# Kernel tuning notes

Hardware: AMD Instinct MI355X
Metric: run time of the kernel (lower is better)

The kernel has to match this reference:

```python
import jax, jax.numpy as jnp
import numpy as np
import math

NBINS = 10
POOL = 8


def setup_inputs() -> dict:
    key = jax.random.key(0)
    x = jax.random.normal(key, (32, 1, 512, 512), dtype=jnp.float32)
    return {"x": x}


def _hog(x):
    # Sobel kernels: (out=2, in=1, 3, 3); channel 0 = horizontal, channel 1 = vertical.
    sob = jnp.array([[1., 0., -1.], [2., 0., -2.], [1., 0., -1.]], dtype=x.dtype)
    w = jnp.stack([sob, sob.T])[:, None, :, :]
    gxy = jax.lax.conv_general_dilated(
        x, w, window_strides=(1, 1), padding=((1, 1), (1, 1)),
        rhs_dilation=(1, 1), dimension_numbers=("NCHW", "OIHW", "NCHW"))
    gx, gy = gxy[:, 0], gxy[:, 1]            # (n, h, w)
    mag = jnp.sqrt(gx * gx + gy * gy)        # gxy.norm(dim=1)
    phase = jnp.arctan2(gx, gy)
    phase_int = phase / math.pi * NBINS
    # torch: out.scatter_(1, floor(phase_int).long() % nbins, mag) on a zero tensor.
    # NOTE: the subsequent out.scatter_add(...) in the source is OUT-OF-PLACE and its
    # result is discarded, so only the floor-bin scatter contributes. Reproduced faithfully.
    bins = jnp.mod(jnp.floor(phase_int).astype(jnp.int32), NBINS)  # (n, h, w), in [0, nbins)
    onehot = bins[:, None, :, :] == jnp.arange(NBINS, dtype=jnp.int32)[None, :, None, None]
    out = jnp.where(onehot, mag[:, None, :, :], jnp.zeros((), dtype=x.dtype))  # (n, nbins, h, w)
    # AvgPool2d(pool=8, stride=8, padding=0): h, w divisible by POOL.
    n, nb, h, wd = out.shape
    pooled = out.reshape(n, nb, h // POOL, POOL, wd // POOL, POOL).mean(axis=(3, 5))
    return pooled


def reference(x):
    # Original forward runs under torch.no_grad(); mirror with stop_gradient.
    return _hog(jax.lax.stop_gradient(x))
```

## Files before the change

kernel.cpp:

```cpp
#include <hip/hip_runtime.h>


namespace {
constexpr int H = 512, W = 512, NB = 10;
}

typedef __attribute__((ext_vector_type(2))) float f32x2;

__device__ __forceinline__ f32x2 vfma2(f32x2 a, f32x2 b, f32x2 c) {
#if __has_builtin(__builtin_elementwise_fma)
    return __builtin_elementwise_fma(a, b, c);
#else
    f32x2 r; r.x = fmaf(a.x, b.x, c.x); r.y = fmaf(a.y, b.y, c.y); return r;
#endif
}

__device__ __forceinline__ void load_row(const float* __restrict__ img,
                                         int ry, int x0, bool lok, bool rok,
                                         float (&R)[10]) {
    if (ry >= 0 && ry < H) {
        const float* p = img + (size_t)ry * W + x0;
        R[0] = lok ? p[-1] : 0.0f;
        const float4 a = *reinterpret_cast<const float4*>(p);
        const float4 b = *reinterpret_cast<const float4*>(p + 4);
        R[1] = a.x; R[2] = a.y; R[3] = a.z; R[4] = a.w;
        R[5] = b.x; R[6] = b.y; R[7] = b.z; R[8] = b.w;
        R[9] = rok ? p[8] : 0.0f;
    } else {
#pragma unroll
        for (int i = 0; i < 10; ++i) R[i] = 0.0f;
    }
}

__global__ __launch_bounds__(256) void hog_kernel(const float* __restrict__ xin,
                                                  float* __restrict__ out) {
    const int tid  = threadIdx.x;
    const int wid  = (blockIdx.x << 2) + (tid >> 6);
    const int lane = tid & 63;

    const int c   = lane >> 2;
    const int sub = lane & 3;

    const int cg  = (wid << 4) + c;
    const int n   = cg >> 12;
    const int rem = cg & 4095;
    const int ph  = rem >> 6;
    const int pw  = rem & 63;

    const int x0 = pw * 8;
    const int yb = ph * 8 + sub * 2;

    const float* img = xin + (size_t)n * H * W;
    const bool lok = (pw > 0), rok = (pw < 63);

    const float PI32 = 3.14159274101257324f;
    const float C10  = __fmul_rn(__fdiv_rn(1.0f, PI32), 10.0f);

    const float P0 =  3.1826723f, P1 = -1.0513758f, P2 = 0.5734066f,
                P3 = -0.2709868f, P4 =  0.0663202f;
    const float EPSW = 1.25e-4f;

    f32x2 acc2[5];
#pragma unroll
    for (int p = 0; p < 5; ++p) acc2[p] = (f32x2){0.0f, 0.0f};

    auto deposit = [&](int b, float v) {
        const bool  hi = b >= 5;
        const int   q5 = hi ? (b - 5) : b;
        const f32x2 P  = hi ? (f32x2){0.0f, v} : (f32x2){v, 0.0f};
#pragma unroll
        for (int p = 0; p < 5; ++p) {
            const float g = (q5 == p) ? 1.0f : 0.0f;
            acc2[p] = vfma2(P, (f32x2){g, g}, acc2[p]);
        }
    };

    auto process_row = [&](const float (&T)[10], const float (&M)[10],
                           const float (&B)[10]) {
        float S[10], D[10];
#pragma unroll
        for (int i = 0; i < 10; ++i) {
            S[i] = fmaf(2.0f, M[i], T[i]) + B[i];
            D[i] = T[i] - B[i];
        }
#pragma unroll
        for (int j = 0; j < 8; ++j) {
            const float gx = S[j] - S[j + 2];
            const float gy = fmaf(2.0f, D[j + 1], D[j] + D[j + 2]);

            const float mag = __builtin_amdgcn_sqrtf(gx * gx + gy * gy);

            const float ax  = fabsf(gx);
            const float ay  = __uint_as_float(__float_as_uint(gy) ^
                                              (__float_as_uint(gx) & 0x80000000u));
            const float aay = fabsf(ay);

            const bool  q   = ax > aay;
            const float den = q ? ax : aay;
            const float num = q ? ay : ax;
            const float t   = num * __builtin_amdgcn_rcpf(den);
            const float u   = t * t;
            float p = fmaf(P4, u, P3);
            p = fmaf(p, u, P2);
            p = fmaf(p, u, P1);
            p = fmaf(p, u, P0);
            const float s = t * p;
            const float w = q ? (5.0f - s) : ((ay > 0.0f) ? s : (10.0f - s));

            const float dist = fabsf(w - rintf(w));
            const bool flagged = !(dist >= EPSW);

            int   bi;
            float dep;
            if (!flagged) {
                bi  = (int)w;
                dep = mag;
            } else {
                const float t0 = T[j], t1 = T[j + 1], t2 = T[j + 2];
                const float m0 = M[j],                 m2 = M[j + 2];
                const float b0 = B[j], b1 = B[j + 1], b2 = B[j + 2];
                const float gxs = ((((t0 - t2) + 2.0f * m0) - 2.0f * m2) + b0) - b2;
                const float gys = ((((t0 + 2.0f * t1) + t2) - b0) - 2.0f * b1) - b2;
                const float mgs = __builtin_amdgcn_sqrtf(gxs * gxs + gys * gys);

                const float phs = atan2f(gxs, gys);
                const float w10 = __fmul_rn(phs, C10);
                bi = (int)floorf(w10);
                bi %= 10;
                if (bi < 0) bi += 10;
                float half = 0.0f;
                const float rk  = rintf(w10);
                const float eps = fmaxf(4.0f * fabsf(w10) * 1.1920929e-7f, 1.5e-6f);
                if (fabsf(w10 - rk) < eps && mgs < 4.6f) {
                    const int k  = (int)rk;
                    int kb = k % 10;       if (kb < 0) kb += 10;
                    int ka = (k - 1) % 10; if (ka < 0) ka += 10;
                    const int balt = (bi == kb) ? ka : kb;
                    half = 0.5f * mgs;
                    deposit(balt, half);
                }
                dep = mgs - half;
            }

            deposit(bi, dep);
        }
    };

    float R0[10], R1[10], R2[10], R3[10];
    load_row(img, yb - 1, x0, lok, rok, R0);
    load_row(img, yb,     x0, lok, rok, R1);
    load_row(img, yb + 1, x0, lok, rok, R2);
    load_row(img, yb + 2, x0, lok, rok, R3);
    process_row(R0, R1, R2);
    process_row(R1, R2, R3);

    float v0 = 0.0f, v1 = 0.0f, v2 = 0.0f, v3 = 0.0f, v4 = 0.0f;
#pragma unroll
    for (int p = 0; p < 5; ++p) {
        float sx = acc2[p].x, sy = acc2[p].y;
        sx += __shfl_xor(sx, 1, 64);
        sx += __shfl_xor(sx, 2, 64);
        sy += __shfl_xor(sy, 1, 64);
        sy += __shfl_xor(sy, 2, 64);
        const float vq = (sub & 1) ? sy : sx;
        v0 = (p == 0) ? vq : v0;
        v1 = (p == 1) ? vq : v1;
        v2 = (p == 2) ? vq : v2;
        v3 = (p == 3) ? vq : v3;
        v4 = (p == 4) ? vq : v4;
    }

    if (sub < 2) {
        const float inv = 1.0f / 64.0f;
        const size_t obase = (((size_t)n * NB) * 64 + (size_t)ph) * 64 + (size_t)pw
                           + (size_t)sub * 5 * 4096;
        out[obase]            = v0 * inv;
        out[obase + 1 * 4096] = v1 * inv;
        out[obase + 2 * 4096] = v2 * inv;
        out[obase + 3 * 4096] = v3 * inv;
        out[obase + 4 * 4096] = v4 * inv;
    }
}

extern "C" void kernel_launch(void* const* d_in, const int* in_sizes, int n_in,
                              void* d_out, int out_size, void* d_ws, size_t ws_size,
                              hipStream_t stream) {
    const float* x = (const float*)d_in[0];
    float* out = (float*)d_out;
    hipLaunchKernelGGL(hog_kernel, dim3(2048), dim3(256), 0, stream, x, out);
}
```

Measured before the change: 21.10 us.

## Assign one full 8x8 pooling cell per thread with rolling row buffers

```diff
diff --git a/kernel.cpp b/kernel.cpp
--- a/kernel.cpp
+++ b/kernel.cpp
@@ -38,17 +38,14 @@
     const int wid  = (blockIdx.x << 2) + (tid >> 6);
     const int lane = tid & 63;
 
-    const int c   = lane >> 2;
-    const int sub = lane & 3;
-
-    const int cg  = (wid << 4) + c;
+    const int cg  = (wid << 6) + lane;
     const int n   = cg >> 12;
     const int rem = cg & 4095;
     const int ph  = rem >> 6;
     const int pw  = rem & 63;
 
     const int x0 = pw * 8;
-    const int yb = ph * 8 + sub * 2;
+    const int y0 = ph * 8;
 
     const float* img = xin + (size_t)n * H * W;
     const bool lok = (pw > 0), rok = (pw < 63);
@@ -146,39 +143,32 @@
         }
     };
 
-    float R0[10], R1[10], R2[10], R3[10];
-    load_row(img, yb - 1, x0, lok, rok, R0);
-    load_row(img, yb,     x0, lok, rok, R1);
-    load_row(img, yb + 1, x0, lok, rok, R2);
-    load_row(img, yb + 2, x0, lok, rok, R3);
-    process_row(R0, R1, R2);
-    process_row(R1, R2, R3);
+    float A[10], B[10], C[10], D[10];
+    load_row(img, y0 - 1, x0, lok, rok, A);
+    load_row(img, y0,     x0, lok, rok, B);
+    load_row(img, y0 + 1, x0, lok, rok, C);
+    process_row(A, B, C);
+    load_row(img, y0 + 2, x0, lok, rok, D);
+    process_row(B, C, D);
+    load_row(img, y0 + 3, x0, lok, rok, A);
+    process_row(C, D, A);
+    load_row(img, y0 + 4, x0, lok, rok, B);
+    process_row(D, A, B);
+    load_row(img, y0 + 5, x0, lok, rok, C);
+    process_row(A, B, C);
+    load_row(img, y0 + 6, x0, lok, rok, D);
+    process_row(B, C, D);
+    load_row(img, y0 + 7, x0, lok, rok, A);
+    process_row(C, D, A);
+    load_row(img, y0 + 8, x0, lok, rok, B);
+    process_row(D, A, B);
 
-    float v0 = 0.0f, v1 = 0.0f, v2 = 0.0f, v3 = 0.0f, v4 = 0.0f;
+    const float inv = 1.0f / 64.0f;
+    const size_t obase = (((size_t)n * NB) * 64 + (size_t)ph) * 64 + (size_t)pw;
 #pragma unroll
     for (int p = 0; p < 5; ++p) {
-        float sx = acc2[p].x, sy = acc2[p].y;
-        sx += __shfl_xor(sx, 1, 64);
-        sx += __shfl_xor(sx, 2, 64);
-        sy += __shfl_xor(sy, 1, 64);
-        sy += __shfl_xor(sy, 2, 64);
-        const float vq = (sub & 1) ? sy : sx;
-        v0 = (p == 0) ? vq : v0;
-        v1 = (p == 1) ? vq : v1;
-        v2 = (p == 2) ? vq : v2;
-        v3 = (p == 3) ? vq : v3;
-        v4 = (p == 4) ? vq : v4;
-    }
-
-    if (sub < 2) {
-        const float inv = 1.0f / 64.0f;
-        const size_t obase = (((size_t)n * NB) * 64 + (size_t)ph) * 64 + (size_t)pw
-                           + (size_t)sub * 5 * 4096;
-        out[obase]            = v0 * inv;
-        out[obase + 1 * 4096] = v1 * inv;
-        out[obase + 2 * 4096] = v2 * inv;
-        out[obase + 3 * 4096] = v3 * inv;
-        out[obase + 4 * 4096] = v4 * inv;
+        out[obase + (size_t)p * 4096]       = acc2[p].x * inv;
+        out[obase + (size_t)(p + 5) * 4096] = acc2[p].y * inv;
     }
 }
 
@@ -187,5 +177,5 @@
                               hipStream_t stream) {
     const float* x = (const float*)d_in[0];
     float* out = (float*)d_out;
-    hipLaunchKernelGGL(hog_kernel, dim3(2048), dim3(256), 0, stream, x, out);
+    hipLaunchKernelGGL(hog_kernel, dim3(512), dim3(256), 0, stream, x, out);
 }
```

Measured after the change: 31.22 us. 1.48x slower.
